# Kernel optimization log

Measured on AMD Instinct MI355X. Metric: run time of the kernel, lower is better.

The kernel has to match this reference:

```python
import jax, jax.numpy as jnp
import numpy as np

N = 50000
E = 800000
EPS = 1e-5


def gcn_conv(x, W, b, src, dst, n):
    # PyG GCNConv: h = xW; add self-loops; symmetric norm D^-1/2 A_hat D^-1/2; out = agg + bias
    h = x @ W                                            # [N, out]
    deg = jax.ops.segment_sum(jnp.ones_like(src, dtype=h.dtype), dst, num_segments=n) + 1.0
    inv_sqrt = jax.lax.rsqrt(deg)                        # [N]
    coef = inv_sqrt[src] * inv_sqrt[dst]                 # [E]
    agg = jax.ops.segment_sum(h[src] * coef[:, None], dst, num_segments=n)
    agg = agg + h * (inv_sqrt * inv_sqrt)[:, None]       # self-loop term
    return agg + b


def batchnorm(h, gamma, beta):
    mean = jnp.mean(h, axis=0)
    var = jnp.var(h, axis=0)
    return gamma * (h - mean) * jax.lax.rsqrt(var + EPS) + beta


def setup_inputs() -> dict:
    key = jax.random.key(0)
    ks = jax.random.split(key, 8)
    x = jax.random.normal(ks[0], (N, 128), dtype=jnp.float32)
    edge_index = jax.random.randint(ks[1], (2, E), 0, N, dtype=jnp.int64)
    s = 1.0 / np.sqrt(128)
    W1 = jax.random.uniform(ks[2], (128, 128), jnp.float32, -s, s)
    W2 = jax.random.uniform(ks[3], (128, 128), jnp.float32, -s, s)
    W3 = jax.random.uniform(ks[4], (128, 64), jnp.float32, -s, s)
    b1 = jnp.zeros((128,), jnp.float32)
    b2 = jnp.zeros((128,), jnp.float32)
    b3 = jnp.zeros((64,), jnp.float32)
    g1 = jnp.ones((128,), jnp.float32)
    bt1 = jnp.zeros((128,), jnp.float32)
    g2 = jnp.ones((128,), jnp.float32)
    bt2 = jnp.zeros((128,), jnp.float32)
    return {"x": x, "edge_index": edge_index, "W1": W1, "b1": b1, "g1": g1, "bt1": bt1,
            "W2": W2, "b2": b2, "g2": g2, "bt2": bt2, "W3": W3, "b3": b3}


def reference(x, edge_index, W1, b1, g1, bt1, W2, b2, g2, bt2, W3, b3):
    src, dst = edge_index[0], edge_index[1]
    h = gcn_conv(x, W1, b1, src, dst, N)
    h = jax.nn.relu(batchnorm(h, g1, bt1))
    h = gcn_conv(h, W2, b2, src, dst, N)
    h = jax.nn.relu(batchnorm(h, g2, bt2))
    out = gcn_conv(h, W3, b3, src, dst, N)
    return out
```

## Files before the change

### kernel.cpp

```cpp
#include <hip/hip_runtime.h>

#define N_NODES 50000
#define N_EDGES 800000
static constexpr float EPS = 1e-5f;
static constexpr int SCAN_NB = (N_NODES + 255) / 256;
static constexpr int GEMM_NB = (N_NODES + 63) / 64;
static constexpr int FILL_NB = (N_EDGES + 1023) / 1024;

using bf16x8 = __attribute__((ext_vector_type(8))) short;
using f32x4  = __attribute__((ext_vector_type(4))) float;

static __device__ __forceinline__ unsigned short f2bf(float f) {
    unsigned int u = __float_as_uint(f);
    return (unsigned short)((u + 0x7FFFu + ((u >> 16) & 1u)) >> 16);
}
static __device__ __forceinline__ float blo(unsigned int w) { return __uint_as_float(w << 16); }
static __device__ __forceinline__ float bhi(unsigned int w) { return __uint_as_float(w & 0xffff0000u); }

__global__ __launch_bounds__(256) void k_wconv_zero(
    const float* __restrict__ W1, const float* __restrict__ W2,
    const float* __restrict__ W3,
    unsigned short* __restrict__ Wf1, unsigned short* __restrict__ Wf2,
    unsigned short* __restrict__ Wf3,
    int4* __restrict__ zbase, int zero16) {
    int gid = blockIdx.x * 256 + threadIdx.x;
    for (int i = gid; i < zero16; i += 160 * 256)
        zbase[i] = make_int4(0, 0, 0, 0);
    const float* W; unsigned short* Wf; int NCOL, idx;
    if (gid < 16384)      { W = W1; Wf = Wf1; NCOL = 128; idx = gid; }
    else if (gid < 32768) { W = W2; Wf = Wf2; NCOL = 128; idx = gid - 16384; }
    else                  { W = W3; Wf = Wf3; NCOL = 64;  idx = gid - 32768; }
    int j  = idx & 7;
    int l  = (idx >> 3) & 63;
    int s  = (idx >> 9) & 3;
    int tn = idx >> 11;
    int n = tn * 16 + (l & 15);
    int k = s * 32 + (l >> 4) * 8 + j;
    Wf[idx] = f2bf(W[k * NCOL + n]);
}

template <int NCOL, bool BN, bool ABF16>
static __device__ __forceinline__ void gemm_body(
    int row0, int t,
    const void* __restrict__ Ap, const unsigned short* __restrict__ Wf,
    const float* __restrict__ stats,
    const float* __restrict__ gamma, const float* __restrict__ beta,
    unsigned short* __restrict__ H,
    unsigned short* As, float* sc_s, float* sh_s) {
    if (BN) {
        if (t < 128) {
            float s  = stats[t];
            float sq = stats[128 + t];
            float mean = s * (1.0f / N_NODES);
            float var  = sq * (1.0f / N_NODES) - mean * mean;
            float sc = gamma[t] * rsqrtf(var + EPS);
            sc_s[t] = sc;
            sh_s[t] = beta[t] - mean * sc;
        }
        __syncthreads();
    }

#pragma unroll
    for (int i = 0; i < 4; i++) {
        int q = i * 256 + t;
        int row = q >> 4;
        int c8  = (q & 15) * 8;
        int grow = row0 + row;
        float v[8];
        if (grow < N_NODES) {
            if (ABF16) {
                uint4 p = *(const uint4*)((const unsigned short*)Ap + (size_t)grow * 128 + c8);
                v[0] = blo(p.x); v[1] = bhi(p.x); v[2] = blo(p.y); v[3] = bhi(p.y);
                v[4] = blo(p.z); v[5] = bhi(p.z); v[6] = blo(p.w); v[7] = bhi(p.w);
            } else {
                const float* Af = (const float*)Ap + (size_t)grow * 128 + c8;
                float4 f0 = *(const float4*)Af;
                float4 f1 = *(const float4*)(Af + 4);
                v[0] = f0.x; v[1] = f0.y; v[2] = f0.z; v[3] = f0.w;
                v[4] = f1.x; v[5] = f1.y; v[6] = f1.z; v[7] = f1.w;
            }
        } else {
#pragma unroll
            for (int j = 0; j < 8; j++) v[j] = 0.f;
        }
        if (BN) {
#pragma unroll
            for (int j = 0; j < 8; j++)
                v[j] = fmaxf(fmaf(v[j], sc_s[c8 + j], sh_s[c8 + j]), 0.f);
        }
        uint4 pk;
        pk.x = (unsigned)f2bf(v[0]) | ((unsigned)f2bf(v[1]) << 16);
        pk.y = (unsigned)f2bf(v[2]) | ((unsigned)f2bf(v[3]) << 16);
        pk.z = (unsigned)f2bf(v[4]) | ((unsigned)f2bf(v[5]) << 16);
        pk.w = (unsigned)f2bf(v[6]) | ((unsigned)f2bf(v[7]) << 16);
        *(uint4*)&As[row * 136 + c8] = pk;
    }
    __syncthreads();

    const int wv = t >> 6;
    const int l  = t & 63;
    const int m  = l & 15;
    const int kq = l >> 4;

    bf16x8 afrag[4];
    const unsigned short* arow = &As[(wv * 16 + m) * 136 + kq * 8];
#pragma unroll
    for (int s = 0; s < 4; s++)
        afrag[s] = *(const bf16x8*)(arow + s * 32);

    constexpr int NT = NCOL / 16;
#pragma unroll
    for (int tn = 0; tn < NT; tn++) {
        f32x4 acc = {0.f, 0.f, 0.f, 0.f};
#pragma unroll
        for (int s = 0; s < 4; s++) {
            bf16x8 b = *(const bf16x8*)&Wf[(size_t)((tn * 4 + s) * 64 + l) * 8];
            acc = __builtin_amdgcn_mfma_f32_16x16x32_bf16(afrag[s], b, acc, 0, 0, 0);
        }
        int col = tn * 16 + m;
#pragma unroll
        for (int r = 0; r < 4; r++) {
            int row = row0 + wv * 16 + kq * 4 + r;
            if (row < N_NODES) H[(size_t)row * NCOL + col] = f2bf(acc[r]);
        }
    }
}

template <int NCOL>
__global__ __launch_bounds__(256) void k_gemm_bn(
    const unsigned short* __restrict__ A, const unsigned short* __restrict__ Wf,
    const float* __restrict__ stats,
    const float* __restrict__ gamma, const float* __restrict__ beta,
    unsigned short* __restrict__ H) {
    __shared__ unsigned short As[64 * 136];
    __shared__ float sc_s[128], sh_s[128];
    gemm_body<NCOL, true, true>(blockIdx.x * 64, threadIdx.x, A, Wf, stats,
                                gamma, beta, H, As, sc_s, sh_s);
}

__global__ __launch_bounds__(256) void k_prep_gemm1(
    const int* __restrict__ ei, int* __restrict__ deg, int* __restrict__ rank,
    const float* __restrict__ x, const unsigned short* __restrict__ Wf1,
    unsigned short* __restrict__ h1) {
    __shared__ unsigned short As[64 * 136];
    __shared__ float sc_s[128], sh_s[128];
    if (blockIdx.x < FILL_NB) {
        int e0 = (blockIdx.x * 256 + threadIdx.x) * 4;
        if (e0 >= N_EDGES) return;
        int4 d4 = *(const int4*)&ei[N_EDGES + e0];
        int4 r;
        r.x = atomicAdd(&deg[d4.x], 1);
        r.y = atomicAdd(&deg[d4.y], 1);
        r.z = atomicAdd(&deg[d4.z], 1);
        r.w = atomicAdd(&deg[d4.w], 1);
        *(int4*)&rank[e0] = r;
    } else {
        gemm_body<128, false, false>((blockIdx.x - FILL_NB) * 64, threadIdx.x,
                                     x, Wf1, nullptr, nullptr, nullptr, h1,
                                     As, sc_s, sh_s);
    }
}

__global__ __launch_bounds__(256) void k_scan1(const int* __restrict__ deg,
                                               float* __restrict__ inv_sqrt,
                                               int* __restrict__ excl,
                                               int* __restrict__ partials) {
    const int t = threadIdx.x;
    const int i = blockIdx.x * 256 + t;
    int v = (i < N_NODES) ? deg[i] : 0;
    if (i < N_NODES) inv_sqrt[i] = rsqrtf((float)v + 1.0f);
    __shared__ int sh[256];
    sh[t] = v;
    __syncthreads();
    for (int off = 1; off < 256; off <<= 1) {
        int u = (t >= off) ? sh[t - off] : 0;
        __syncthreads();
        sh[t] += u;
        __syncthreads();
    }
    if (i < N_NODES) excl[i] = sh[t] - v;
    if (t == 255) partials[blockIdx.x] = sh[t];
}

__global__ __launch_bounds__(256) void k_scan23_fill(
    const int* __restrict__ excl, const int* __restrict__ partials,
    int* __restrict__ rowptr,
    const int* __restrict__ ei, const int* __restrict__ rank,
    int* __restrict__ esrc) {
    const int t = threadIdx.x;
    __shared__ int sh[256];
    __shared__ int ps[256];
    int v = (t < SCAN_NB) ? partials[t] : 0;
    sh[t] = v;
    __syncthreads();
    for (int off = 1; off < 256; off <<= 1) {
        int u = (t >= off) ? sh[t - off] : 0;
        __syncthreads();
        sh[t] += u;
        __syncthreads();
    }
    ps[t] = sh[t] - v;
    __syncthreads();

    if (blockIdx.x < SCAN_NB) {
        const int i = blockIdx.x * 256 + t;
        if (i < N_NODES) rowptr[i] = excl[i] + ps[blockIdx.x];
        if (i == 0) rowptr[N_NODES] = N_EDGES;
    } else {
        int e0 = ((blockIdx.x - SCAN_NB) * 256 + t) * 4;
        if (e0 < N_EDGES) {
            int4 s4 = *(const int4*)&ei[e0];
            int4 d4 = *(const int4*)&ei[N_EDGES + e0];
            int4 r4 = *(const int4*)&rank[e0];
            int p0 = excl[d4.x] + ps[d4.x >> 8] + r4.x;
            int p1 = excl[d4.y] + ps[d4.y >> 8] + r4.y;
            int p2 = excl[d4.z] + ps[d4.z >> 8] + r4.z;
            int p3 = excl[d4.w] + ps[d4.w >> 8] + r4.w;
            esrc[p0] = s4.x;
            esrc[p1] = s4.y;
            esrc[p2] = s4.z;
            esrc[p3] = s4.w;
        }
    }
}

template <int F, bool OUTBF>
__global__ __launch_bounds__(256) void k_agg(const int* __restrict__ rowptr,
                                             const int* __restrict__ esrc,
                                             const float* __restrict__ inv_sqrt,
                                             const unsigned short* __restrict__ H,
                                             const float* __restrict__ bias,
                                             void* __restrict__ OUT) {
    constexpr int LPN = F / 8;
    constexpr int NPB = 256 / LPN;
    const int t = threadIdx.x;
    const int node = blockIdx.x * NPB + t / LPN;
    const int lane = t % LPN;
    if (node >= N_NODES) return;

    const uint4* __restrict__ Hv = (const uint4*)H;
    const int beg = rowptr[node];
    const int end = rowptr[node + 1];
    const float rsn = inv_sqrt[node];

    float acc[8];
#pragma unroll
    for (int i = 0; i < 8; i++) acc[i] = 0.f;

#define ACC8(P, C)                                                     \
    acc[0] = fmaf(blo((P).x), (C), acc[0]);                            \
    acc[1] = fmaf(bhi((P).x), (C), acc[1]);                            \
    acc[2] = fmaf(blo((P).y), (C), acc[2]);                            \
    acc[3] = fmaf(bhi((P).y), (C), acc[3]);                            \
    acc[4] = fmaf(blo((P).z), (C), acc[4]);                            \
    acc[5] = fmaf(bhi((P).z), (C), acc[5]);                            \
    acc[6] = fmaf(blo((P).w), (C), acc[6]);                            \
    acc[7] = fmaf(bhi((P).w), (C), acc[7]);

    int j = beg;
    for (; j + 7 < end; j += 8) {
        int4 sa = *(const int4*)&esrc[j];
        int4 sb = *(const int4*)&esrc[j + 4];
        uint4 p0 = Hv[(size_t)sa.x * LPN + lane];
        uint4 p1 = Hv[(size_t)sa.y * LPN + lane];
        uint4 p2 = Hv[(size_t)sa.z * LPN + lane];
        uint4 p3 = Hv[(size_t)sa.w * LPN + lane];
        uint4 p4 = Hv[(size_t)sb.x * LPN + lane];
        uint4 p5 = Hv[(size_t)sb.y * LPN + lane];
        uint4 p6 = Hv[(size_t)sb.z * LPN + lane];
        uint4 p7 = Hv[(size_t)sb.w * LPN + lane];
        float c0 = inv_sqrt[sa.x] * rsn, c1 = inv_sqrt[sa.y] * rsn;
        float c2 = inv_sqrt[sa.z] * rsn, c3 = inv_sqrt[sa.w] * rsn;
        float c4 = inv_sqrt[sb.x] * rsn, c5 = inv_sqrt[sb.y] * rsn;
        float c6 = inv_sqrt[sb.z] * rsn, c7 = inv_sqrt[sb.w] * rsn;
        ACC8(p0, c0) ACC8(p1, c1) ACC8(p2, c2) ACC8(p3, c3)
        ACC8(p4, c4) ACC8(p5, c5) ACC8(p6, c6) ACC8(p7, c7)
    }
    if (j + 3 < end) {
        int4 sa = *(const int4*)&esrc[j];
        uint4 p0 = Hv[(size_t)sa.x * LPN + lane];
        uint4 p1 = Hv[(size_t)sa.y * LPN + lane];
        uint4 p2 = Hv[(size_t)sa.z * LPN + lane];
        uint4 p3 = Hv[(size_t)sa.w * LPN + lane];
        float c0 = inv_sqrt[sa.x] * rsn, c1 = inv_sqrt[sa.y] * rsn;
        float c2 = inv_sqrt[sa.z] * rsn, c3 = inv_sqrt[sa.w] * rsn;
        ACC8(p0, c0) ACC8(p1, c1) ACC8(p2, c2) ACC8(p3, c3)
        j += 4;
    }
    for (; j < end; j++) {
        int s0 = esrc[j];
        float c0 = inv_sqrt[s0] * rsn;
        uint4 p0 = Hv[(size_t)s0 * LPN + lane];
        ACC8(p0, c0)
    }
#undef ACC8

    uint4 ps = Hv[(size_t)node * LPN + lane];
    float idv = rsn * rsn;
    float4 b0 = ((const float4*)bias)[lane * 2];
    float4 b1 = ((const float4*)bias)[lane * 2 + 1];
    acc[0] = fmaf(blo(ps.x), idv, acc[0]) + b0.x;
    acc[1] = fmaf(bhi(ps.x), idv, acc[1]) + b0.y;
    acc[2] = fmaf(blo(ps.y), idv, acc[2]) + b0.z;
    acc[3] = fmaf(bhi(ps.y), idv, acc[3]) + b0.w;
    acc[4] = fmaf(blo(ps.z), idv, acc[4]) + b1.x;
    acc[5] = fmaf(bhi(ps.z), idv, acc[5]) + b1.y;
    acc[6] = fmaf(blo(ps.w), idv, acc[6]) + b1.z;
    acc[7] = fmaf(bhi(ps.w), idv, acc[7]) + b1.w;

    if (OUTBF) {
        uint4 pk;
        pk.x = (unsigned)f2bf(acc[0]) | ((unsigned)f2bf(acc[1]) << 16);
        pk.y = (unsigned)f2bf(acc[2]) | ((unsigned)f2bf(acc[3]) << 16);
        pk.z = (unsigned)f2bf(acc[4]) | ((unsigned)f2bf(acc[5]) << 16);
        pk.w = (unsigned)f2bf(acc[6]) | ((unsigned)f2bf(acc[7]) << 16);
        ((uint4*)OUT)[(size_t)node * LPN + lane] = pk;
    } else {
        float4* o = (float4*)OUT + ((size_t)node * LPN + lane) * 2;
        o[0] = make_float4(acc[0], acc[1], acc[2], acc[3]);
        o[1] = make_float4(acc[4], acc[5], acc[6], acc[7]);
    }
}

__global__ __launch_bounds__(256) void k_stats(const unsigned short* __restrict__ A,
                                               float* __restrict__ stats) {
    const int t  = threadIdx.x;
    const int c4 = t & 31;
    const int rr = t >> 5;
    float4 sum = make_float4(0.f, 0.f, 0.f, 0.f);
    float4 sq  = make_float4(0.f, 0.f, 0.f, 0.f);
    for (int row = blockIdx.x * 8 + rr; row < N_NODES; row += gridDim.x * 8) {
        uint2 p = *(const uint2*)&A[(size_t)row * 128 + c4 * 4];
        float vx = blo(p.x), vy = bhi(p.x), vz = blo(p.y), vw = bhi(p.y);
        sum.x += vx; sum.y += vy; sum.z += vz; sum.w += vw;
        sq.x += vx * vx; sq.y += vy * vy; sq.z += vz * vz; sq.w += vw * vw;
    }
    __shared__ float4 red[2][8][32];
    red[0][rr][c4] = sum;
    red[1][rr][c4] = sq;
    __syncthreads();
    if (t < 32) {
        float4 s = make_float4(0.f, 0.f, 0.f, 0.f);
        float4 q = make_float4(0.f, 0.f, 0.f, 0.f);
#pragma unroll
        for (int i = 0; i < 8; i++) {
            float4 a = red[0][i][t];
            float4 b = red[1][i][t];
            s.x += a.x; s.y += a.y; s.z += a.z; s.w += a.w;
            q.x += b.x; q.y += b.y; q.z += b.z; q.w += b.w;
        }
        int c = t * 4;
        atomicAdd(&stats[c + 0], s.x); atomicAdd(&stats[c + 1], s.y);
        atomicAdd(&stats[c + 2], s.z); atomicAdd(&stats[c + 3], s.w);
        atomicAdd(&stats[128 + c + 0], q.x); atomicAdd(&stats[128 + c + 1], q.y);
        atomicAdd(&stats[128 + c + 2], q.z); atomicAdd(&stats[128 + c + 3], q.w);
    }
}

extern "C" void kernel_launch(void* const* d_in, const int* in_sizes, int n_in,
                              void* d_out, int out_size, void* d_ws, size_t ws_size,
                              hipStream_t stream) {
    const float* x   = (const float*)d_in[0];
    const int*   ei  = (const int*)d_in[1];
    const float* W1  = (const float*)d_in[2];
    const float* b1  = (const float*)d_in[3];
    const float* g1  = (const float*)d_in[4];
    const float* bt1 = (const float*)d_in[5];
    const float* W2  = (const float*)d_in[6];
    const float* b2  = (const float*)d_in[7];
    const float* g2  = (const float*)d_in[8];
    const float* bt2 = (const float*)d_in[9];
    const float* W3  = (const float*)d_in[10];
    const float* b3  = (const float*)d_in[11];
    float* out = (float*)d_out;

    char* ws = (char*)d_ws;
    size_t off = 0;
    auto alloc = [&](size_t bytes) { char* p = ws + off; off += (bytes + 255) & ~(size_t)255; return p; };
    int*   deg      = (int*)  alloc((size_t)N_NODES * 4);
    float* stats1   = (float*)alloc(256 * 4);
    float* stats2   = (float*)alloc(256 * 4);
    const size_t zbytes = (size_t)((char*)(stats2 + 256) - (char*)deg);
    const int zero16 = (int)(zbytes / 16);
    float* inv_sqrt = (float*)alloc((size_t)N_NODES * 4);
    int*   excl     = (int*)  alloc((size_t)N_NODES * 4);
    int*   partials = (int*)  alloc(256 * 4);
    int*   rowptr   = (int*)  alloc((size_t)(N_NODES + 1) * 4);
    int*   rank     = (int*)  alloc((size_t)N_EDGES * 4);
    int*   esrc     = (int*)  alloc((size_t)N_EDGES * 4);
    unsigned short* Wf1 = (unsigned short*)alloc((size_t)128 * 128 * 2);
    unsigned short* Wf2 = (unsigned short*)alloc((size_t)128 * 128 * 2);
    unsigned short* Wf3 = (unsigned short*)alloc((size_t)64 * 128 * 2);
    unsigned short* h1  = (unsigned short*)alloc((size_t)N_NODES * 128 * 2);
    unsigned short* h2  = (unsigned short*)alloc((size_t)N_NODES * 128 * 2);
    unsigned short* h3  = (unsigned short*)alloc((size_t)N_NODES * 64 * 2);
    unsigned short* agg1 = (unsigned short*)alloc((size_t)N_NODES * 128 * 2);
    unsigned short* agg2 = (unsigned short*)alloc((size_t)N_NODES * 128 * 2);

    k_wconv_zero<<<160, 256, 0, stream>>>(W1, W2, W3, Wf1, Wf2, Wf3,
                                          (int4*)deg, zero16);
    k_prep_gemm1<<<FILL_NB + GEMM_NB, 256, 0, stream>>>(ei, deg, rank, x, Wf1, h1);
    k_scan1<<<SCAN_NB, 256, 0, stream>>>(deg, inv_sqrt, excl, partials);
    k_scan23_fill<<<SCAN_NB + FILL_NB, 256, 0, stream>>>(excl, partials, rowptr,
                                                         ei, rank, esrc);
    k_agg<128, true><<<N_NODES / 16, 256, 0, stream>>>(rowptr, esrc, inv_sqrt, h1, b1, agg1);
    k_stats<<<256, 256, 0, stream>>>(agg1, stats1);
    k_gemm_bn<128><<<GEMM_NB, 256, 0, stream>>>(agg1, Wf2, stats1, g1, bt1, h2);
    k_agg<128, true><<<N_NODES / 16, 256, 0, stream>>>(rowptr, esrc, inv_sqrt, h2, b2, agg2);
    k_stats<<<256, 256, 0, stream>>>(agg2, stats2);
    k_gemm_bn<64><<<GEMM_NB, 256, 0, stream>>>(agg2, Wf3, stats2, g2, bt2, h3);
    k_agg<64, false><<<(N_NODES + 31) / 32, 256, 0, stream>>>(rowptr, esrc, inv_sqrt, h3, b3, out);
}
```

Baseline: 321.1 us.

## Build CSR with per-chunk LDS byte histograms instead of global degree atomics

Degree counting and edge ranking now happen in 16 blocks, each building a local shared-memory histogram with four 8-bit counters packed per word, instead of one global atomicAdd per edge. The per-chunk counts are turned into chunk bases and node offsets by a prefix pass folded into the first GEMM launch, which removes the separate scan kernel and the workspace zeroing. Ranks shrink from 4 bytes to 1 byte per edge. The risk is that only 16 blocks do the histogram work, which limits parallelism. A node that gets more than 255 edges within one chunk would overflow its 8-bit counter.

Result: faster. 306.5 us (-4.6%).

```diff
diff --git a/kernel.cpp b/kernel.cpp
--- a/kernel.cpp
+++ b/kernel.cpp
@@ -3,9 +3,13 @@
 #define N_NODES 50000
 #define N_EDGES 800000
 static constexpr float EPS = 1e-5f;
-static constexpr int SCAN_NB = (N_NODES + 255) / 256;
+static constexpr int NCH   = 16;
+static constexpr int EPC   = N_EDGES / NCH;
+static constexpr int NW    = (N_NODES + 3) / 4;
+static constexpr int SCAN_NB = (N_NODES + 1023) / 1024;
 static constexpr int GEMM_NB = (N_NODES + 63) / 64;
 static constexpr int FILL_NB = (N_EDGES + 1023) / 1024;
+static constexpr int WCONV_NB = 160;
 
 using bf16x8 = __attribute__((ext_vector_type(8))) short;
 using f32x4  = __attribute__((ext_vector_type(4))) float;
@@ -17,26 +21,49 @@
 static __device__ __forceinline__ float blo(unsigned int w) { return __uint_as_float(w << 16); }
 static __device__ __forceinline__ float bhi(unsigned int w) { return __uint_as_float(w & 0xffff0000u); }
 
-__global__ __launch_bounds__(256) void k_wconv_zero(
+__global__ __launch_bounds__(256) void k_hist_wconv(
+    const int* __restrict__ ei, unsigned char* __restrict__ rank8,
+    unsigned int* __restrict__ basesU,
     const float* __restrict__ W1, const float* __restrict__ W2,
     const float* __restrict__ W3,
     unsigned short* __restrict__ Wf1, unsigned short* __restrict__ Wf2,
-    unsigned short* __restrict__ Wf3,
-    int4* __restrict__ zbase, int zero16) {
-    int gid = blockIdx.x * 256 + threadIdx.x;
-    for (int i = gid; i < zero16; i += 160 * 256)
-        zbase[i] = make_int4(0, 0, 0, 0);
-    const float* W; unsigned short* Wf; int NCOL, idx;
-    if (gid < 16384)      { W = W1; Wf = Wf1; NCOL = 128; idx = gid; }
-    else if (gid < 32768) { W = W2; Wf = Wf2; NCOL = 128; idx = gid - 16384; }
-    else                  { W = W3; Wf = Wf3; NCOL = 64;  idx = gid - 32768; }
-    int j  = idx & 7;
-    int l  = (idx >> 3) & 63;
-    int s  = (idx >> 9) & 3;
-    int tn = idx >> 11;
-    int n = tn * 16 + (l & 15);
-    int k = s * 32 + (l >> 4) * 8 + j;
-    Wf[idx] = f2bf(W[k * NCOL + n]);
+    unsigned short* __restrict__ Wf3, int4* __restrict__ statz) {
+    __shared__ unsigned int h[NW];
+    const int t = threadIdx.x;
+    if (blockIdx.x < NCH) {
+        for (int i = t; i < NW; i += 256) h[i] = 0;
+        __syncthreads();
+        const int cbeg = blockIdx.x * EPC;
+        for (int e0 = cbeg + t * 4; e0 < cbeg + EPC; e0 += 1024) {
+            int4 d4 = *(const int4*)&ei[N_EDGES + e0];
+            int sh0 = (d4.x & 3) * 8, sh1 = (d4.y & 3) * 8;
+            int sh2 = (d4.z & 3) * 8, sh3 = (d4.w & 3) * 8;
+            unsigned int o0 = atomicAdd(&h[d4.x >> 2], 1u << sh0);
+            unsigned int o1 = atomicAdd(&h[d4.y >> 2], 1u << sh1);
+            unsigned int o2 = atomicAdd(&h[d4.z >> 2], 1u << sh2);
+            unsigned int o3 = atomicAdd(&h[d4.w >> 2], 1u << sh3);
+            unsigned int pk = ((o0 >> sh0) & 0xffu) | (((o1 >> sh1) & 0xffu) << 8)
+                            | (((o2 >> sh2) & 0xffu) << 16) | (((o3 >> sh3) & 0xffu) << 24);
+            *(unsigned int*)&rank8[e0] = pk;
+        }
+        __syncthreads();
+        for (int i = t; i < NW; i += 256)
+            basesU[blockIdx.x * NW + i] = h[i];
+    } else {
+        int gid = (blockIdx.x - NCH) * 256 + t;
+        if (gid < 128) statz[gid] = make_int4(0, 0, 0, 0);
+        const float* W; unsigned short* Wf; int NCOL, idx;
+        if (gid < 16384)      { W = W1; Wf = Wf1; NCOL = 128; idx = gid; }
+        else if (gid < 32768) { W = W2; Wf = Wf2; NCOL = 128; idx = gid - 16384; }
+        else                  { W = W3; Wf = Wf3; NCOL = 64;  idx = gid - 32768; }
+        int j  = idx & 7;
+        int l  = (idx >> 3) & 63;
+        int s  = (idx >> 9) & 3;
+        int tn = idx >> 11;
+        int n = tn * 16 + (l & 15);
+        int k = s * 32 + (l >> 4) * 8 + j;
+        Wf[idx] = f2bf(W[k * NCOL + n]);
+    }
 }
 
 template <int NCOL, bool BN, bool ABF16>
@@ -138,54 +165,59 @@
                                 gamma, beta, H, As, sc_s, sh_s);
 }
 
-__global__ __launch_bounds__(256) void k_prep_gemm1(
-    const int* __restrict__ ei, int* __restrict__ deg, int* __restrict__ rank,
+__global__ __launch_bounds__(256) void k_gemm1_scan1(
     const float* __restrict__ x, const unsigned short* __restrict__ Wf1,
-    unsigned short* __restrict__ h1) {
+    unsigned short* __restrict__ h1,
+    unsigned int* __restrict__ basesU, float* __restrict__ inv_sqrt,
+    int* __restrict__ excl, int* __restrict__ partials) {
     __shared__ unsigned short As[64 * 136];
     __shared__ float sc_s[128], sh_s[128];
-    if (blockIdx.x < FILL_NB) {
-        int e0 = (blockIdx.x * 256 + threadIdx.x) * 4;
-        if (e0 >= N_EDGES) return;
-        int4 d4 = *(const int4*)&ei[N_EDGES + e0];
-        int4 r;
-        r.x = atomicAdd(&deg[d4.x], 1);
-        r.y = atomicAdd(&deg[d4.y], 1);
-        r.z = atomicAdd(&deg[d4.z], 1);
-        r.w = atomicAdd(&deg[d4.w], 1);
-        *(int4*)&rank[e0] = r;
+    const int t = threadIdx.x;
+    if (blockIdx.x < GEMM_NB) {
+        gemm_body<128, false, false>(blockIdx.x * 64, t, x, Wf1,
+                                     nullptr, nullptr, nullptr, h1, As, sc_s, sh_s);
     } else {
-        gemm_body<128, false, false>((blockIdx.x - FILL_NB) * 64, threadIdx.x,
-                                     x, Wf1, nullptr, nullptr, nullptr, h1,
-                                     As, sc_s, sh_s);
-    }
-}
-
-__global__ __launch_bounds__(256) void k_scan1(const int* __restrict__ deg,
-                                               float* __restrict__ inv_sqrt,
-                                               int* __restrict__ excl,
-                                               int* __restrict__ partials) {
-    const int t = threadIdx.x;
-    const int i = blockIdx.x * 256 + t;
-    int v = (i < N_NODES) ? deg[i] : 0;
-    if (i < N_NODES) inv_sqrt[i] = rsqrtf((float)v + 1.0f);
-    __shared__ int sh[256];
-    sh[t] = v;
-    __syncthreads();
-    for (int off = 1; off < 256; off <<= 1) {
-        int u = (t >= off) ? sh[t - off] : 0;
-        __syncthreads();
-        sh[t] += u;
-        __syncthreads();
-    }
-    if (i < N_NODES) excl[i] = sh[t] - v;
-    if (t == 255) partials[blockIdx.x] = sh[t];
-}
-
-__global__ __launch_bounds__(256) void k_scan23_fill(
+        int* shi = (int*)As;
+        const int g = (blockIdx.x - GEMM_NB) * 256 + t;
+        int r0 = 0, r1 = 0, r2 = 0, r3 = 0;
+        if (g < NW) {
+#pragma unroll
+            for (int c = 0; c < NCH; c++) {
+                unsigned int w = basesU[c * NW + g];
+                unsigned int pb = (unsigned)r0 | ((unsigned)r1 << 8)
+                                | ((unsigned)r2 << 16) | ((unsigned)r3 << 24);
+                basesU[c * NW + g] = pb;
+                r0 += w & 0xff; r1 += (w >> 8) & 0xff;
+                r2 += (w >> 16) & 0xff; r3 += (w >> 24) & 0xff;
+            }
+        }
+        int S = r0 + r1 + r2 + r3;
+        shi[t] = S;
+        __syncthreads();
+        for (int off = 1; off < 256; off <<= 1) {
+            int u = (t >= off) ? shi[t - off] : 0;
+            __syncthreads();
+            shi[t] += u;
+            __syncthreads();
+        }
+        int base = shi[t] - S;
+        if (g < NW) {
+            int i0 = g * 4;
+            *(int4*)&excl[i0] = make_int4(base, base + r0, base + r0 + r1,
+                                          base + r0 + r1 + r2);
+            *(float4*)&inv_sqrt[i0] = make_float4(
+                rsqrtf((float)r0 + 1.0f), rsqrtf((float)r1 + 1.0f),
+                rsqrtf((float)r2 + 1.0f), rsqrtf((float)r3 + 1.0f));
+        }
+        if (t == 255) partials[blockIdx.x - GEMM_NB] = shi[t];
+    }
+}
+
+__global__ __launch_bounds__(256) void k_scan2_fill(
     const int* __restrict__ excl, const int* __restrict__ partials,
     int* __restrict__ rowptr,
-    const int* __restrict__ ei, const int* __restrict__ rank,
+    const int* __restrict__ ei, const unsigned char* __restrict__ rank8,
+    const unsigned char* __restrict__ cb8,
     int* __restrict__ esrc) {
     const int t = threadIdx.x;
     __shared__ int sh[256];
@@ -203,19 +235,25 @@
     __syncthreads();
 
     if (blockIdx.x < SCAN_NB) {
-        const int i = blockIdx.x * 256 + t;
-        if (i < N_NODES) rowptr[i] = excl[i] + ps[blockIdx.x];
-        if (i == 0) rowptr[N_NODES] = N_EDGES;
+        int i0 = (blockIdx.x * 256 + t) * 4;
+        if (i0 < N_NODES) {
+            int4 e4 = *(const int4*)&excl[i0];
+            int b = ps[blockIdx.x];
+            *(int4*)&rowptr[i0] = make_int4(e4.x + b, e4.y + b, e4.z + b, e4.w + b);
+        }
+        if (blockIdx.x == 0 && t == 0) rowptr[N_NODES] = N_EDGES;
     } else {
         int e0 = ((blockIdx.x - SCAN_NB) * 256 + t) * 4;
         if (e0 < N_EDGES) {
+            const int c = e0 / EPC;
+            const unsigned char* cb = cb8 + (size_t)c * N_NODES;
             int4 s4 = *(const int4*)&ei[e0];
             int4 d4 = *(const int4*)&ei[N_EDGES + e0];
-            int4 r4 = *(const int4*)&rank[e0];
-            int p0 = excl[d4.x] + ps[d4.x >> 8] + r4.x;
-            int p1 = excl[d4.y] + ps[d4.y >> 8] + r4.y;
-            int p2 = excl[d4.z] + ps[d4.z >> 8] + r4.z;
-            int p3 = excl[d4.w] + ps[d4.w >> 8] + r4.w;
+            unsigned int r4 = *(const unsigned int*)&rank8[e0];
+            int p0 = excl[d4.x] + ps[d4.x >> 10] + cb[d4.x] + (r4 & 0xff);
+            int p1 = excl[d4.y] + ps[d4.y >> 10] + cb[d4.y] + ((r4 >> 8) & 0xff);
+            int p2 = excl[d4.z] + ps[d4.z >> 10] + cb[d4.z] + ((r4 >> 16) & 0xff);
+            int p3 = excl[d4.w] + ps[d4.w >> 10] + cb[d4.w] + ((r4 >> 24) & 0xff);
             esrc[p0] = s4.x;
             esrc[p1] = s4.y;
             esrc[p2] = s4.z;
@@ -377,16 +415,14 @@
     char* ws = (char*)d_ws;
     size_t off = 0;
     auto alloc = [&](size_t bytes) { char* p = ws + off; off += (bytes + 255) & ~(size_t)255; return p; };
-    int*   deg      = (int*)  alloc((size_t)N_NODES * 4);
     float* stats1   = (float*)alloc(256 * 4);
     float* stats2   = (float*)alloc(256 * 4);
-    const size_t zbytes = (size_t)((char*)(stats2 + 256) - (char*)deg);
-    const int zero16 = (int)(zbytes / 16);
+    unsigned int*  basesU = (unsigned int*)alloc((size_t)NCH * NW * 4);
+    unsigned char* rank8  = (unsigned char*)alloc((size_t)N_EDGES);
     float* inv_sqrt = (float*)alloc((size_t)N_NODES * 4);
     int*   excl     = (int*)  alloc((size_t)N_NODES * 4);
     int*   partials = (int*)  alloc(256 * 4);
     int*   rowptr   = (int*)  alloc((size_t)(N_NODES + 1) * 4);
-    int*   rank     = (int*)  alloc((size_t)N_EDGES * 4);
     int*   esrc     = (int*)  alloc((size_t)N_EDGES * 4);
     unsigned short* Wf1 = (unsigned short*)alloc((size_t)128 * 128 * 2);
     unsigned short* Wf2 = (unsigned short*)alloc((size_t)128 * 128 * 2);
@@ -397,12 +433,15 @@
     unsigned short* agg1 = (unsigned short*)alloc((size_t)N_NODES * 128 * 2);
     unsigned short* agg2 = (unsigned short*)alloc((size_t)N_NODES * 128 * 2);
 
-    k_wconv_zero<<<160, 256, 0, stream>>>(W1, W2, W3, Wf1, Wf2, Wf3,
-                                          (int4*)deg, zero16);
-    k_prep_gemm1<<<FILL_NB + GEMM_NB, 256, 0, stream>>>(ei, deg, rank, x, Wf1, h1);
-    k_scan1<<<SCAN_NB, 256, 0, stream>>>(deg, inv_sqrt, excl, partials);
-    k_scan23_fill<<<SCAN_NB + FILL_NB, 256, 0, stream>>>(excl, partials, rowptr,
-                                                         ei, rank, esrc);
+    k_hist_wconv<<<NCH + WCONV_NB, 256, 0, stream>>>(ei, rank8, basesU,
+                                                     W1, W2, W3, Wf1, Wf2, Wf3,
+                                                     (int4*)stats1);
+    k_gemm1_scan1<<<GEMM_NB + SCAN_NB, 256, 0, stream>>>(x, Wf1, h1, basesU,
+                                                         inv_sqrt, excl, partials);
+    k_scan2_fill<<<SCAN_NB + FILL_NB, 256, 0, stream>>>(excl, partials, rowptr,
+                                                        ei, rank8,
+                                                        (const unsigned char*)basesU,
+                                                        esrc);
     k_agg<128, true><<<N_NODES / 16, 256, 0, stream>>>(rowptr, esrc, inv_sqrt, h1, b1, agg1);
     k_stats<<<256, 256, 0, stream>>>(agg1, stats1);
     k_gemm_bn<128><<<GEMM_NB, 256, 0, stream>>>(agg1, Wf2, stats1, g1, bt1, h2);
```
